# Performance work log

Measured on AMD Instinct MI355X. Metric: run time of the kernel, lower is better.

Reference implementation:

```python
import math
import jax, jax.numpy as jnp
import numpy as np

B, N, D = 16, 4096, 256
N_CAT, N_TPC, N_VPT, N_SP = 16, 8, 4, 16
N_TYPE = N_CAT * N_TPC          # 128
N_VAR = N_TYPE * N_VPT          # 512
THRESH = 0.1
MASK_VAL = jnp.finfo(jnp.float32).min / 2


def _linear(x, w, b):
    # torch nn.Linear: y = x @ W^T + b, W: (out, in)
    return x @ w.T + b


def _level(codes, proj_w, proj_b, K, X, mask, tau):
    """One codebook level: attention of codes over tokens.
    codes: (M, d). Returns H:(B,M,d), w_raw:(B,M)."""
    Q = _linear(codes, proj_w, proj_b)                       # (M, d)
    attn = jnp.einsum('md,bnd->bmn', Q, K) / math.sqrt(D)    # (B, M, N)
    attn = jnp.where(mask[:, None, :], attn, MASK_VAL)
    attn = jnp.clip(attn, -50.0, 50.0)
    G = jnp.nan_to_num(jax.nn.softmax(attn, axis=-1))        # (B, M, N)
    H = jnp.einsum('bmn,bnd->bmd', G, X)                     # (B, M, d)
    w_raw = jnp.linalg.norm(H, axis=-1) / tau                # (B, M)
    return H, w_raw


def _sparsify(w, thr):
    ws = jnp.where(w > thr, w, 0.0)
    return ws / (ws.sum(axis=-1, keepdims=True) + 1e-8)


def _forward(X, positions, category_codes, type_codes, variant_codes,
             spatial_codes, log_tau, cat_w, cat_b, type_w, type_b,
             var_w, var_b, sp_w, sp_b, k_w, k_b, g1_w, g1_b, g2_w, g2_b,
             out_w, out_b, ln_g, ln_b, level_weights, mask):
    tau = jnp.clip(jnp.exp(log_tau[0]) + 0.1, 0.1, 2.0)
    K = _linear(X, k_w, k_b)                                 # (B, N, d)

    # Level 0: category
    H_cat, w_cat_raw = _level(category_codes, cat_w, cat_b, K, X, mask, tau)
    w_cat = jax.nn.softmax(w_cat_raw, axis=-1)
    w_cat_sp = _sparsify(w_cat, THRESH)

    # Level 1: type, gated by category selection
    H_type, w_type_raw = _level(type_codes.reshape(-1, D), type_w, type_b,
                                K, X, mask, tau)
    w_t = (w_type_raw.reshape(-1, N_CAT, N_TPC) * w_cat_sp[:, :, None]
           ).reshape(-1, N_TYPE)
    w_type = jax.nn.softmax(w_t, axis=-1)
    w_type_sp = _sparsify(w_type, THRESH / 2)

    # Level 2: variant, gated by type selection
    H_var, w_var_raw = _level(variant_codes.reshape(-1, D), var_w, var_b,
                              K, X, mask, tau)
    w_type_exp = jnp.repeat(w_type_sp, N_VPT, axis=-1)       # (B, 512)
    w_var = jax.nn.softmax(w_var_raw * w_type_exp, axis=-1)
    w_var_sp = _sparsify(w_var, THRESH / 4)

    # Spatial level (independent)
    H_sp, w_sp_raw = _level(spatial_codes, sp_w, sp_b, K, X, mask, tau)
    w_sp = jax.nn.softmax(w_sp_raw, axis=-1)
    w_sp_sp = _sparsify(w_sp, THRESH)

    z_cat = jnp.einsum('bm,bmd->bd', w_cat_sp, H_cat)
    z_type = jnp.einsum('bm,bmd->bd', w_type_sp, H_type)
    z_var = jnp.einsum('bm,bmd->bd', w_var_sp, H_var)
    z_spatial = jnp.einsum('bm,bmd->bd', w_sp_sp, H_sp)

    # Position gating of category summary
    mask_f = mask.astype(X.dtype)[:, :, None]
    pos_pooled = (positions * mask_f).sum(1) / jnp.maximum(mask_f.sum(1), 1.0)
    gate_in = jnp.concatenate([z_cat, pos_pooled], axis=-1)  # (B, 2d)
    h = jax.nn.gelu(_linear(gate_in, g1_w, g1_b), approximate=False)
    pos_gate = jax.nn.sigmoid(_linear(h, g2_w, g2_b))
    z_cat = z_cat * pos_gate

    # Learned level combine + gated output projection
    lw = jax.nn.softmax(level_weights)
    z = (lw[0] * z_cat + lw[1] * z_type + lw[2] * z_var + lw[3] * z_spatial)
    z = _linear(z, out_w, out_b)
    mu = z.mean(-1, keepdims=True)
    var = z.var(-1, keepdims=True)
    z = (z - mu) / jnp.sqrt(var + 1e-5) * ln_g + ln_b
    return z


def setup_inputs() -> dict:
    key = jax.random.key(0)
    ks = jax.random.split(key, 32)
    s = 1.0 / math.sqrt(D)
    inp = {
        'X': jax.random.normal(ks[0], (B, N, D), jnp.float32),
        'positions': jax.random.normal(ks[1], (B, N, D), jnp.float32),
        'category_codes': jax.random.normal(ks[2], (N_CAT, D)) * 0.02,
        'type_codes': jax.random.normal(ks[3], (N_CAT, N_TPC, D)) * 0.02,
        'variant_codes': jax.random.normal(ks[4], (N_CAT, N_TPC, N_VPT, D)) * 0.02,
        'spatial_codes': jax.random.normal(ks[5], (N_SP, D)) * 0.02,
        'log_tau': jnp.zeros((1,), jnp.float32),
        'cat_w': jax.random.normal(ks[6], (D, D)) * s,
        'cat_b': jnp.zeros((D,)),
        'type_w': jax.random.normal(ks[7], (D, D)) * s,
        'type_b': jnp.zeros((D,)),
        'var_w': jax.random.normal(ks[8], (D, D)) * s,
        'var_b': jnp.zeros((D,)),
        'sp_w': jax.random.normal(ks[9], (D, D)) * s,
        'sp_b': jnp.zeros((D,)),
        'k_w': jax.random.normal(ks[10], (D, D)) * s,
        'k_b': jnp.zeros((D,)),
        'g1_w': jax.random.normal(ks[11], (D, 2 * D)) * s,
        'g1_b': jnp.zeros((D,)),
        'g2_w': jax.random.normal(ks[12], (D, D)) * s,
        'g2_b': jnp.zeros((D,)),
        'out_w': jax.random.normal(ks[13], (D, D)) * s,
        'out_b': jnp.zeros((D,)),
        'ln_g': jnp.ones((D,)),
        'ln_b': jnp.zeros((D,)),
        'level_weights': jnp.ones((4,)) / 4.0,
        'mask': jnp.ones((B, N), jnp.bool_),
    }
    return inp


def reference(X, positions, category_codes, type_codes, variant_codes,
              spatial_codes, log_tau, cat_w, cat_b, type_w, type_b,
              var_w, var_b, sp_w, sp_b, k_w, k_b, g1_w, g1_b, g2_w, g2_b,
              out_w, out_b, ln_g, ln_b, level_weights, mask):
    return _forward(X, positions, category_codes, type_codes, variant_codes,
                    spatial_codes, log_tau, cat_w, cat_b, type_w, type_b,
                    var_w, var_b, sp_w, sp_b, k_w, k_b, g1_w, g1_b,
                    g2_w, g2_b, out_w, out_b, ln_g, ln_b, level_weights, mask)
```

## Files before the change

### kernel.cpp

```cpp
#include <hip/hip_runtime.h>


#define DEV static __device__ __forceinline__

typedef short bf16x8 __attribute__((ext_vector_type(8)));
typedef float f32x4 __attribute__((ext_vector_type(4)));
typedef unsigned short u16x8 __attribute__((ext_vector_type(8)));

DEV float bf2f(unsigned short u) {
  return __uint_as_float(((unsigned int)u) << 16);
}
DEV unsigned short f2bf(float f) {
  unsigned int x = __float_as_uint(f);
  unsigned int r = (x + 0x7fffu + ((x >> 16) & 1u)) >> 16;
  return (unsigned short)r;
}

DEV void gl2lds16(const void* g, void* l) {
  __builtin_amdgcn_global_load_lds(
      (const __attribute__((address_space(1))) unsigned int*)g,
      (__attribute__((address_space(3))) unsigned int*)l, 16, 0, 0);
}

DEV bf16x8 pack8(const float4 a, const float4 b) {
  bf16x8 r;
  r[0] = (short)f2bf(a.x); r[1] = (short)f2bf(a.y);
  r[2] = (short)f2bf(a.z); r[3] = (short)f2bf(a.w);
  r[4] = (short)f2bf(b.x); r[5] = (short)f2bf(b.y);
  r[6] = (short)f2bf(b.z); r[7] = (short)f2bf(b.w);
  return r;
}

DEV size_t pk_off(int rt, int ks) { return ((size_t)rt * 8 + ks) * 512; }

__global__ __launch_bounds__(256) void fused_pre(
    const float* __restrict__ X, const float* __restrict__ k_w,
    const float* __restrict__ k_b, unsigned short* __restrict__ Kp,
    unsigned short* __restrict__ XTp, const float* __restrict__ positions,
    const unsigned char* __restrict__ mask, float* __restrict__ ppart,
    float* __restrict__ cpart, const float* __restrict__ cat_codes,
    const float* __restrict__ type_codes, const float* __restrict__ var_codes,
    const float* __restrict__ sp_codes, const float* __restrict__ cat_w,
    const float* __restrict__ cat_b, const float* __restrict__ type_w,
    const float* __restrict__ type_b, const float* __restrict__ var_w,
    const float* __restrict__ var_b, const float* __restrict__ sp_w,
    const float* __restrict__ sp_b, unsigned short* __restrict__ Qp) {
  __shared__ __align__(16) char smem[36864];
  const int g = blockIdx.x;
  const int t = threadIdx.x;

  if (g < 1024) {
    unsigned short* As = (unsigned short*)smem;
    unsigned short* Bs = (unsigned short*)(smem + 18432);
    const int m0 = (g >> 1) * 128, c0 = (g & 1) * 128;
    const int l = t & 63, w = t >> 6;
    const int wm = (w & 1) * 64, wn = (w >> 1) * 64;
    const f32x4 zero = {0.f, 0.f, 0.f, 0.f};
    f32x4 acc[4][4];
#pragma unroll
    for (int i = 0; i < 4; ++i)
#pragma unroll
      for (int j = 0; j < 4; ++j) acc[i][j] = zero;
    const int rr = t >> 3, cc = (t & 7) * 8;
    for (int kc = 0; kc < 256; kc += 64) {
      __syncthreads();
#pragma unroll
      for (int p = 0; p < 4; ++p) {
        const int r = p * 32 + rr;
        const float* xs = &X[(size_t)(m0 + r) * 256 + kc + cc];
        const float4 a0 = *(const float4*)&xs[0];
        const float4 a1 = *(const float4*)&xs[4];
        *(bf16x8*)&As[r * 72 + cc] = pack8(a0, a1);
        const float* wsrc = &k_w[(size_t)(c0 + r) * 256 + kc + cc];
        const float4 b0 = *(const float4*)&wsrc[0];
        const float4 b1 = *(const float4*)&wsrc[4];
        *(bf16x8*)&Bs[r * 72 + cc] = pack8(b0, b1);
      }
      __syncthreads();
#pragma unroll
      for (int ks = 0; ks < 2; ++ks) {
        const int koff = ks * 32 + ((l >> 4) & 3) * 8;
        bf16x8 a[4], b[4];
#pragma unroll
        for (int f = 0; f < 4; ++f)
          a[f] = *(const bf16x8*)&As[(wm + f * 16 + (l & 15)) * 72 + koff];
#pragma unroll
        for (int f = 0; f < 4; ++f)
          b[f] = *(const bf16x8*)&Bs[(wn + f * 16 + (l & 15)) * 72 + koff];
#pragma unroll
        for (int i = 0; i < 4; ++i)
#pragma unroll
          for (int j = 0; j < 4; ++j)
            acc[i][j] = __builtin_amdgcn_mfma_f32_16x16x32_bf16(
                a[i], b[j], acc[i][j], 0, 0, 0);
      }
    }
    const int q = (l >> 4) & 3;
#pragma unroll
    for (int j = 0; j < 4; ++j) {
      const int c = c0 + wn + j * 16 + (l & 15);
      const float bv = k_b[c];
#pragma unroll
      for (int i = 0; i < 4; ++i) {
        const int mrow = m0 + wm + i * 16 + q * 4;
#pragma unroll
        for (int r = 0; r < 4; ++r) {
          const int m = mrow + r;
          Kp[pk_off(m >> 4, c >> 5) + ((m & 15) + 16 * ((c >> 3) & 3)) * 8 +
             (c & 7)] = f2bf(acc[i][j][r] + bv);
        }
      }
    }
  } else if (g < 5120) {
    float (*Ls)[65] = (float (*)[65])smem;
    const int gg = g - 1024;
    const int b = gg >> 8;
    const int td = (gg >> 6) & 3;
    const int tn = gg & 63;
    const int nl = t >> 2, dp = (t & 3) * 16;
    const float* src =
        X + ((size_t)b * 4096 + tn * 64 + nl) * 256 + td * 64 + dp;
#pragma unroll
    for (int v = 0; v < 4; ++v) {
      const float4 x = *(const float4*)&src[v * 4];
      Ls[nl][dp + v * 4 + 0] = x.x;
      Ls[nl][dp + v * 4 + 1] = x.y;
      Ls[nl][dp + v * 4 + 2] = x.z;
      Ls[nl][dp + v * 4 + 3] = x.w;
    }
    __syncthreads();
    const int dl = t >> 2, np = (t & 3) * 16;
    u16x8 h0, h1;
#pragma unroll
    for (int j = 0; j < 8; ++j) h0[j] = f2bf(Ls[np + j][dl]);
#pragma unroll
    for (int j = 0; j < 8; ++j) h1[j] = f2bf(Ls[np + 8 + j][dl]);
    const int d = td * 64 + dl;
    const int n0g = tn * 64 + np;
    const int n1g = n0g + 8;
    unsigned short* dst = XTp + (size_t)b * 1048576;
    const size_t o0 = (((size_t)(d >> 4) * 128) + (n0g >> 5)) * 512 +
                      ((d & 15) + 16 * ((n0g >> 3) & 3)) * 8;
    const size_t o1 = (((size_t)(d >> 4) * 128) + (n1g >> 5)) * 512 +
                      ((d & 15) + 16 * ((n1g >> 3) & 3)) * 8;
    *(u16x8*)&dst[o0] = h0;
    *(u16x8*)&dst[o1] = h1;
  } else if (g < 5632) {
    float4* red4 = (float4*)smem;
    float* redc = (float*)(smem + 4096);
    const int gg = g - 5120;
    const int b = gg >> 5, seg = gg & 31;
    const int dg = t & 63;
    const int nl = t >> 6;
    const int n0 = seg * 128;
    float4 acc = make_float4(0.f, 0.f, 0.f, 0.f);
    float c = 0.f;
    const float* pb = positions + (size_t)b * 4096 * 256;
    for (int j = 0; j < 32; ++j) {
      const int n = n0 + j * 4 + nl;
      const float mf = mask[(size_t)b * 4096 + n] ? 1.f : 0.f;
      const float4 v = *(const float4*)&pb[(size_t)n * 256 + dg * 4];
      acc.x = fmaf(mf, v.x, acc.x);
      acc.y = fmaf(mf, v.y, acc.y);
      acc.z = fmaf(mf, v.z, acc.z);
      acc.w = fmaf(mf, v.w, acc.w);
      c += mf;
    }
    red4[t] = acc;
    if (dg == 0) redc[nl] = c;
    __syncthreads();
    if (t < 64) {
      float4 s = red4[t];
      const float4 s1 = red4[t + 64], s2 = red4[t + 128], s3 = red4[t + 192];
      s.x += s1.x + s2.x + s3.x;
      s.y += s1.y + s2.y + s3.y;
      s.z += s1.z + s2.z + s3.z;
      s.w += s1.w + s2.w + s3.w;
      *(float4*)&ppart[(size_t)(b * 32 + seg) * 256 + t * 4] = s;
      if (t == 0) cpart[b * 32 + seg] = redc[0] + redc[1] + redc[2] + redc[3];
    }
  } else {
    float* xs = (float*)smem;
    const int m = g - 5632;
    const size_t off = pk_off(m >> 4, t >> 5) +
                       ((m & 15) + 16 * ((t >> 3) & 3)) * 8 + (t & 7);
    if (m >= 672) {
      Qp[off] = 0;
      return;
    }
    const float* code;
    const float* W;
    const float* bias;
    if (m < 16)       { code = cat_codes  + m * 256;         W = cat_w;  bias = cat_b; }
    else if (m < 144) { code = type_codes + (m - 16) * 256;  W = type_w; bias = type_b; }
    else if (m < 656) { code = var_codes  + (m - 144) * 256; W = var_w;  bias = var_b; }
    else              { code = sp_codes   + (m - 656) * 256; W = sp_w;   bias = sp_b; }
    xs[t] = code[t];
    __syncthreads();
    float a = bias[t];
    const float* wr = W + (size_t)t * 256;
    for (int k = 0; k < 256; k += 4) {
      const float4 w = *(const float4*)&wr[k];
      a = fmaf(w.x, xs[k], a);
      a = fmaf(w.y, xs[k + 1], a);
      a = fmaf(w.z, xs[k + 2], a);
      a = fmaf(w.w, xs[k + 3], a);
    }
    Qp[off] = f2bf(a);
  }
}

__global__ __launch_bounds__(256, 2) void attn_fused(
    const unsigned short* __restrict__ Qp, const unsigned short* __restrict__ Kp,
    const unsigned short* __restrict__ XTp,
    const unsigned char* __restrict__ mask, float* __restrict__ H2,
    float* __restrict__ lsum2) {
  __shared__ __align__(16) unsigned short Ks[2][16384];
  __shared__ __align__(16) unsigned short Plds[64 * 72];
  __shared__ unsigned char msk[2048];
  const int combo = blockIdx.x;
  const int m0 = blockIdx.y * 64;
  const int b = combo >> 1;
  const int nsl = combo & 1;
  const int nbase = nsl * 2048;
  const int t = threadIdx.x, l = t & 63, w = t >> 6;
  const int l15 = l & 15, q = l >> 4;
  ((uint2*)msk)[t] = ((const uint2*)(mask + (size_t)b * 4096 + nbase))[t];
  const int mt_g = (m0 >> 4) + w;
  bf16x8 qf[8];
#pragma unroll
  for (int ks = 0; ks < 8; ++ks)
    qf[ks] = *(const bf16x8*)&Qp[pk_off(mt_g, ks) + l * 8];
  const f32x4 zero = {0.f, 0.f, 0.f, 0.f};
  f32x4 accO[4][4];
#pragma unroll
  for (int i = 0; i < 4; ++i)
#pragma unroll
    for (int j = 0; j < 4; ++j) accO[i][j] = zero;
  f32x4 rs = zero;
  const unsigned short* XTb = XTp + (size_t)b * 1048576;
  const unsigned short* Kchunk0 = Kp + ((size_t)b * 256 + (nbase >> 4)) * 4096;
#pragma unroll
  for (int i = 0; i < 8; ++i)
    gl2lds16(Kchunk0 + (w * 8 + i) * 512 + l * 8, &Ks[0][(w * 8 + i) * 512]);
  for (int c = 0; c < 32; ++c) {
    const int cur = c & 1;
    __syncthreads();
    const int nst0 = (nbase >> 5) + c * 2;
    bf16x8 xf[2][4];
#pragma unroll
    for (int ks2 = 0; ks2 < 2; ++ks2)
#pragma unroll
      for (int dj = 0; dj < 4; ++dj)
        xf[ks2][dj] = *(const bf16x8*)&XTb[((size_t)(4 * w + dj) * 128 +
                                            nst0 + ks2) * 512 + l * 8];
    f32x4 accS[4];
#pragma unroll
    for (int f = 0; f < 4; ++f) accS[f] = zero;
#pragma unroll
    for (int ks = 0; ks < 8; ++ks) {
      bf16x8 kf[4];
#pragma unroll
      for (int f = 0; f < 4; ++f)
        kf[f] = *(const bf16x8*)&Ks[cur][(f * 8 + ks) * 512 + l * 8];
#pragma unroll
      for (int f = 0; f < 4; ++f)
        accS[f] = __builtin_amdgcn_mfma_f32_16x16x32_bf16(qf[ks], kf[f],
                                                          accS[f], 0, 0, 0);
    }
#pragma unroll
    for (int f = 0; f < 4; ++f) {
      const bool mk = msk[c * 64 + f * 16 + l15] != 0;
#pragma unroll
      for (int r = 0; r < 4; ++r) {
        float s = accS[f][r] * 0.0625f;
        s = fminf(fmaxf(s, -50.f), 50.f);
        if (!mk) s = -50.f;
        const float e = __expf(s);
        Plds[(w * 16 + q * 4 + r) * 72 + f * 16 + l15] = f2bf(e);
        rs[r] += e;
      }
    }
    __syncthreads();
    if (c < 31) {
      const unsigned short* src = Kchunk0 + (size_t)(c + 1) * 16384;
      unsigned short* dst = &Ks[1 - cur][0];
#pragma unroll
      for (int i = 0; i < 8; ++i)
        gl2lds16(src + (w * 8 + i) * 512 + l * 8, dst + (w * 8 + i) * 512);
    }
#pragma unroll
    for (int ks2 = 0; ks2 < 2; ++ks2) {
      bf16x8 pf[4];
#pragma unroll
      for (int mt = 0; mt < 4; ++mt)
        pf[mt] = *(const bf16x8*)&Plds[(mt * 16 + l15) * 72 + ks2 * 32 + q * 8];
#pragma unroll
      for (int mt = 0; mt < 4; ++mt)
#pragma unroll
        for (int dj = 0; dj < 4; ++dj)
          accO[mt][dj] = __builtin_amdgcn_mfma_f32_16x16x32_bf16(
              pf[mt], xf[ks2][dj], accO[mt][dj], 0, 0, 0);
    }
  }
  float* lpart = lsum2 + (size_t)(nsl * 16 + b) * 672;
#pragma unroll
  for (int r = 0; r < 4; ++r) {
    float v = rs[r];
    v += __shfl_xor(v, 1, 64);
    v += __shfl_xor(v, 2, 64);
    v += __shfl_xor(v, 4, 64);
    v += __shfl_xor(v, 8, 64);
    const int m = m0 + w * 16 + q * 4 + r;
    if (l15 == 0 && m < 672) lpart[m] = v;
  }
  float* Hpart = H2 + (size_t)(nsl * 16 + b) * 672 * 256;
#pragma unroll
  for (int mt = 0; mt < 4; ++mt) {
    const int mbase = m0 + mt * 16 + q * 4;
#pragma unroll
    for (int dj = 0; dj < 4; ++dj) {
      const int d = w * 64 + dj * 16 + l15;
#pragma unroll
      for (int r = 0; r < 4; ++r) {
        const int m = mbase + r;
        if (m < 672) Hpart[(size_t)m * 256 + d] = accO[mt][dj][r];
      }
    }
  }
}

__global__ __launch_bounds__(256) void hnorm_kern(
    const float* __restrict__ H2, const float* __restrict__ lsum2,
    const float* __restrict__ log_tau, float* __restrict__ linv,
    float* __restrict__ wraw) {
  const int b = blockIdx.x, j = blockIdx.y;
  const int t = threadIdx.x, l = t & 63, w = t >> 6;
  const int m = j * 4 + w;
  const size_t r0 = ((size_t)b * 672 + m) * 256;
  const size_t r1 = ((size_t)(16 + b) * 672 + m) * 256;
  const float4 v0 = *(const float4*)&H2[r0 + l * 4];
  const float4 v1 = *(const float4*)&H2[r1 + l * 4];
  const float sx = v0.x + v1.x, sy = v0.y + v1.y;
  const float sz = v0.z + v1.z, sw = v0.w + v1.w;
  float ss = sx * sx + sy * sy + sz * sz + sw * sw;
#pragma unroll
  for (int s = 1; s < 64; s <<= 1) ss += __shfl_xor(ss, s, 64);
  if (l == 0) {
    const float lt = lsum2[b * 672 + m] + lsum2[(16 + b) * 672 + m];
    const float li = 1.0f / lt;
    const float tau = fminf(fmaxf(expf(log_tau[0]) + 0.1f, 0.1f), 2.0f);
    linv[b * 672 + m] = li;
    wraw[b * 672 + m] = sqrtf(ss) * li / tau;
  }
}

DEV float wave_max(float v) {
#pragma unroll
  for (int m = 1; m < 64; m <<= 1) v = fmaxf(v, __shfl_xor(v, m, 64));
  return v;
}
DEV float wave_sum(float v) {
#pragma unroll
  for (int m = 1; m < 64; m <<= 1) v += __shfl_xor(v, m, 64);
  return v;
}

__global__ __launch_bounds__(256) void combine_kern(
    const float* __restrict__ wraw, const float* __restrict__ linv,
    const float* __restrict__ H2, float* __restrict__ zpart) {
  const int b = blockIdx.x, j = blockIdx.y, t = threadIdx.x, l = t & 63;
  __shared__ float wr[672];
  __shared__ float wsp[672];
  for (int i = t; i < 672; i += 256) wr[i] = wraw[b * 672 + i];
  __syncthreads();
  {
    const float v = (l < 16) ? wr[l] : -1e30f;
    const float mx = wave_max(v);
    const float e = (l < 16) ? expf(wr[l] - mx) : 0.f;
    const float s = wave_sum(e);
    float ww = e / s;
    ww = (ww > 0.1f) ? ww : 0.f;
    const float s2 = wave_sum(ww);
    if (l < 16) wsp[l] = ww / (s2 + 1e-8f);
  }
  __syncthreads();
  {
    const float L0 = wr[16 + l] * wsp[l >> 3];
    const float L1 = wr[16 + 64 + l] * wsp[(64 + l) >> 3];
    const float mx = wave_max(fmaxf(L0, L1));
    const float e0 = expf(L0 - mx), e1 = expf(L1 - mx);
    const float s = wave_sum(e0 + e1);
    float w0 = e0 / s, w1 = e1 / s;
    w0 = (w0 > 0.05f) ? w0 : 0.f;
    w1 = (w1 > 0.05f) ? w1 : 0.f;
    const float s2 = wave_sum(w0 + w1);
    const float inv2 = 1.f / (s2 + 1e-8f);
    wsp[16 + l] = w0 * inv2;
    wsp[16 + 64 + l] = w1 * inv2;
  }
  __syncthreads();
  {
    float Lv[8];
    float lm = -1e30f;
#pragma unroll
    for (int jj = 0; jj < 8; ++jj) {
      const int i = l * 8 + jj;
      Lv[jj] = wr[144 + i] * wsp[16 + (i >> 2)];
      lm = fmaxf(lm, Lv[jj]);
    }
    const float mx = wave_max(lm);
    float ls = 0.f;
#pragma unroll
    for (int jj = 0; jj < 8; ++jj) {
      Lv[jj] = expf(Lv[jj] - mx);
      ls += Lv[jj];
    }
    const float s = wave_sum(ls);
    const float inv = 1.f / s;
    float ls2 = 0.f;
#pragma unroll
    for (int jj = 0; jj < 8; ++jj) {
      float ww = Lv[jj] * inv;
      ww = (ww > 0.025f) ? ww : 0.f;
      Lv[jj] = ww;
      ls2 += ww;
    }
    const float s2 = wave_sum(ls2);
    const float inv2 = 1.f / (s2 + 1e-8f);
#pragma unroll
    for (int jj = 0; jj < 8; ++jj) wsp[144 + l * 8 + jj] = Lv[jj] * inv2;
  }
  __syncthreads();
  {
    const float v = (l < 16) ? wr[656 + l] : -1e30f;
    const float mx = wave_max(v);
    const float e = (l < 16) ? expf(wr[656 + l] - mx) : 0.f;
    const float s = wave_sum(e);
    float ww = e / s;
    ww = (ww > 0.1f) ? ww : 0.f;
    const float s2 = wave_sum(ww);
    if (l < 16) wsp[656 + l] = ww / (s2 + 1e-8f);
  }
  __syncthreads();
  for (int i = t; i < 672; i += 256) wsp[i] *= linv[b * 672 + i];
  __syncthreads();
  const float* Ha = H2 + (size_t)b * 672 * 256;
  const float* Hc = H2 + (size_t)(16 + b) * 672 * 256;
  const int s0 = j * 84, s1 = s0 + 84;
  const int Llo[4] = {0, 16, 144, 656};
  const int Lhi[4] = {16, 144, 656, 672};
#pragma unroll
  for (int lv = 0; lv < 4; ++lv) {
    const int lo = max(s0, Llo[lv]);
    const int hi = min(s1, Lhi[lv]);
    float z = 0.f;
    for (int m = lo; m < hi; ++m)
      z = fmaf(wsp[m], Ha[(size_t)m * 256 + t] + Hc[(size_t)m * 256 + t], z);
    zpart[(((size_t)b * 8 + j) * 4 + lv) * 256 + t] = z;
  }
}

__global__ __launch_bounds__(1024) void gate_kern(
    const float* __restrict__ zpart, const float* __restrict__ ppart,
    const float* __restrict__ cpart, const float* __restrict__ g1_w,
    const float* __restrict__ g1_b, const float* __restrict__ g2_w,
    const float* __restrict__ g2_b, const float* __restrict__ out_w,
    const float* __restrict__ out_b, const float* __restrict__ ln_g,
    const float* __restrict__ ln_b, const float* __restrict__ lvlw,
    float* __restrict__ out) {
  const int b = blockIdx.x, t = threadIdx.x;
  __shared__ float gin[512];
  __shared__ float zvs[4][256];
  __shared__ float hb[256];
  __shared__ float zc[256];
  __shared__ float oar[256];
  __shared__ float red[256];
  __shared__ float par[1024];
  __shared__ float cred;
  {
    const int lv = t >> 8, tt = t & 255;
    float z = 0.f;
#pragma unroll
    for (int jj = 0; jj < 8; ++jj)
      z += zpart[(((size_t)b * 8 + jj) * 4 + lv) * 256 + tt];
    zvs[lv][tt] = z;
  }
  if (t == 0) {
    float c = 0.f;
    for (int seg = 0; seg < 32; ++seg) c += cpart[b * 32 + seg];
    cred = fmaxf(c, 1.0f);
  }
  __syncthreads();
  if (t < 256) {
    float pa = 0.f;
    for (int seg = 0; seg < 32; ++seg)
      pa += ppart[(size_t)(b * 32 + seg) * 256 + t];
    gin[256 + t] = pa / cred;
    gin[t] = zvs[0][t];
  }
  __syncthreads();
  {
    const int r = t >> 2, p = t & 3;
    const float* w1 = g1_w + (size_t)r * 512 + p * 128;
    const float* gv = gin + p * 128;
    float a = 0.f;
    for (int k = 0; k < 128; k += 4) {
      const float4 w = *(const float4*)&w1[k];
      a = fmaf(w.x, gv[k], a);
      a = fmaf(w.y, gv[k + 1], a);
      a = fmaf(w.z, gv[k + 2], a);
      a = fmaf(w.w, gv[k + 3], a);
    }
    par[t] = a;
  }
  __syncthreads();
  if (t < 256) {
    const float a =
        par[t * 4] + par[t * 4 + 1] + par[t * 4 + 2] + par[t * 4 + 3] +
        g1_b[t];
    hb[t] = 0.5f * a * (1.0f + erff(a * 0.7071067811865475f));
  }
  __syncthreads();
  {
    const int r = t >> 2, p = t & 3;
    const float* w2 = g2_w + (size_t)r * 256 + p * 64;
    const float* hv = hb + p * 64;
    float a = 0.f;
    for (int k = 0; k < 64; k += 4) {
      const float4 w = *(const float4*)&w2[k];
      a = fmaf(w.x, hv[k], a);
      a = fmaf(w.y, hv[k + 1], a);
      a = fmaf(w.z, hv[k + 2], a);
      a = fmaf(w.w, hv[k + 3], a);
    }
    par[t] = a;
  }
  __syncthreads();
  if (t < 256) {
    const float a2 =
        par[t * 4] + par[t * 4 + 1] + par[t * 4 + 2] + par[t * 4 + 3] +
        g2_b[t];
    const float pg = 1.0f / (1.0f + expf(-a2));
    const float l0 = lvlw[0], l1 = lvlw[1], l2 = lvlw[2], l3 = lvlw[3];
    const float mx = fmaxf(fmaxf(l0, l1), fmaxf(l2, l3));
    const float e0 = expf(l0 - mx), e1 = expf(l1 - mx);
    const float e2 = expf(l2 - mx), e3 = expf(l3 - mx);
    const float einv = 1.0f / (e0 + e1 + e2 + e3);
    zc[t] = (e0 * zvs[0][t] * pg + e1 * zvs[1][t] + e2 * zvs[2][t] +
             e3 * zvs[3][t]) *
            einv;
  }
  __syncthreads();
  {
    const int r = t >> 2, p = t & 3;
    const float* wo = out_w + (size_t)r * 256 + p * 64;
    const float* zv = zc + p * 64;
    float a = 0.f;
    for (int k = 0; k < 64; k += 4) {
      const float4 w = *(const float4*)&wo[k];
      a = fmaf(w.x, zv[k], a);
      a = fmaf(w.y, zv[k + 1], a);
      a = fmaf(w.z, zv[k + 2], a);
      a = fmaf(w.w, zv[k + 3], a);
    }
    par[t] = a;
  }
  __syncthreads();
  if (t < 256) {
    const float o =
        par[t * 4] + par[t * 4 + 1] + par[t * 4 + 2] + par[t * 4 + 3] +
        out_b[t];
    oar[t] = o;
    red[t] = o;
  }
  __syncthreads();
  for (int s = 128; s > 0; s >>= 1) {
    if (t < s) red[t] += red[t + s];
    __syncthreads();
  }
  const float mu = red[0] / 256.f;
  __syncthreads();
  if (t < 256) red[t] = oar[t] * oar[t];
  __syncthreads();
  for (int s = 128; s > 0; s >>= 1) {
    if (t < s) red[t] += red[t + s];
    __syncthreads();
  }
  if (t < 256) {
    const float var = red[0] / 256.f - mu * mu;
    out[b * 256 + t] = (oar[t] - mu) * rsqrtf(var + 1e-5f) * ln_g[t] + ln_b[t];
  }
}

extern "C" void kernel_launch(void* const* d_in, const int* in_sizes, int n_in,
                              void* d_out, int out_size, void* d_ws,
                              size_t ws_size, hipStream_t stream) {
  (void)in_sizes; (void)n_in; (void)out_size; (void)ws_size;
  const float* X          = (const float*)d_in[0];
  const float* positions  = (const float*)d_in[1];
  const float* cat_codes  = (const float*)d_in[2];
  const float* type_codes = (const float*)d_in[3];
  const float* var_codes  = (const float*)d_in[4];
  const float* sp_codes   = (const float*)d_in[5];
  const float* log_tau    = (const float*)d_in[6];
  const float* cat_w      = (const float*)d_in[7];
  const float* cat_b      = (const float*)d_in[8];
  const float* type_w     = (const float*)d_in[9];
  const float* type_b     = (const float*)d_in[10];
  const float* var_w      = (const float*)d_in[11];
  const float* var_b      = (const float*)d_in[12];
  const float* sp_w       = (const float*)d_in[13];
  const float* sp_b       = (const float*)d_in[14];
  const float* k_w        = (const float*)d_in[15];
  const float* k_b        = (const float*)d_in[16];
  const float* g1_w       = (const float*)d_in[17];
  const float* g1_b       = (const float*)d_in[18];
  const float* g2_w       = (const float*)d_in[19];
  const float* g2_b       = (const float*)d_in[20];
  const float* out_w      = (const float*)d_in[21];
  const float* out_b      = (const float*)d_in[22];
  const float* ln_g       = (const float*)d_in[23];
  const float* ln_b       = (const float*)d_in[24];
  const float* lvlw       = (const float*)d_in[25];
  const unsigned char* mask = (const unsigned char*)d_in[26];

  char* ws = (char*)d_ws;
  constexpr size_t O_KP  = 0;
  constexpr size_t O_XT  = 33554432;
  constexpr size_t O_QP  = 67108864;
  constexpr size_t O_H2  = 67469312;
  constexpr size_t O_L2  = 89489408;
  constexpr size_t O_PP  = 89575424;
  constexpr size_t O_CP  = 90099712;
  constexpr size_t O_ZP  = 90101760;
  constexpr size_t O_LI  = 90626048;
  constexpr size_t O_WR  = 90669056;

  unsigned short* Kp  = (unsigned short*)(ws + O_KP);
  unsigned short* XTp = (unsigned short*)(ws + O_XT);
  unsigned short* Qp  = (unsigned short*)(ws + O_QP);
  float* H2           = (float*)(ws + O_H2);
  float* lsum2        = (float*)(ws + O_L2);
  float* ppart        = (float*)(ws + O_PP);
  float* cpart        = (float*)(ws + O_CP);
  float* zpart        = (float*)(ws + O_ZP);
  float* linv         = (float*)(ws + O_LI);
  float* wraw         = (float*)(ws + O_WR);
  float* out          = (float*)d_out;

  fused_pre<<<dim3(6336), 256, 0, stream>>>(
      X, k_w, k_b, Kp, XTp, positions, mask, ppart, cpart, cat_codes,
      type_codes, var_codes, sp_codes, cat_w, cat_b, type_w, type_b, var_w,
      var_b, sp_w, sp_b, Qp);

  attn_fused<<<dim3(32, 11), 256, 0, stream>>>(Qp, Kp, XTp, mask, H2, lsum2);

  hnorm_kern<<<dim3(16, 168), 256, 0, stream>>>(H2, lsum2, log_tau, linv,
                                                wraw);

  combine_kern<<<dim3(16, 8), 256, 0, stream>>>(wraw, linv, H2, zpart);

  gate_kern<<<dim3(16), 1024, 0, stream>>>(zpart, ppart, cpart, g1_w, g1_b,
                                           g2_w, g2_b, out_w, out_b, ln_g,
                                           ln_b, lvlw, out);
}
```

Baseline: 383.0 us.

## Load K-projection operands directly to registers; widen combine grid; parallelize ppart reduction

The K-projection GEMM branch of fused_pre drops its LDS staging and barriers: each lane now reads its MFMA fragments straight from global memory and converts them to bf16 in registers. The shared buffer shrinks to match, which may allow more blocks per CU. combine_kern runs 32 slices per batch instead of 8, with the zpart buffer and workspace offsets enlarged to fit. gate_kern now splits the ppart reduction across all 1024 threads. The price is redundant global reads across waves in the GEMM and more partial sums to reduce afterwards.

```diff
diff --git a/kernel.cpp b/kernel.cpp
--- a/kernel.cpp
+++ b/kernel.cpp
@@ -45,60 +45,49 @@
     const float* __restrict__ type_b, const float* __restrict__ var_w,
     const float* __restrict__ var_b, const float* __restrict__ sp_w,
     const float* __restrict__ sp_b, unsigned short* __restrict__ Qp) {
-  __shared__ __align__(16) char smem[36864];
+  __shared__ __align__(16) char smem[16640];
   const int g = blockIdx.x;
   const int t = threadIdx.x;
 
   if (g < 1024) {
-    unsigned short* As = (unsigned short*)smem;
-    unsigned short* Bs = (unsigned short*)(smem + 18432);
     const int m0 = (g >> 1) * 128, c0 = (g & 1) * 128;
     const int l = t & 63, w = t >> 6;
     const int wm = (w & 1) * 64, wn = (w >> 1) * 64;
+    const int l15 = l & 15, q8 = ((l >> 4) & 3) * 8;
+    const float* ax[4];
+    const float* bx[4];
+#pragma unroll
+    for (int f = 0; f < 4; ++f) {
+      ax[f] = X + (size_t)(m0 + wm + f * 16 + l15) * 256;
+      bx[f] = k_w + (size_t)(c0 + wn + f * 16 + l15) * 256;
+    }
     const f32x4 zero = {0.f, 0.f, 0.f, 0.f};
     f32x4 acc[4][4];
 #pragma unroll
     for (int i = 0; i < 4; ++i)
 #pragma unroll
       for (int j = 0; j < 4; ++j) acc[i][j] = zero;
-    const int rr = t >> 3, cc = (t & 7) * 8;
-    for (int kc = 0; kc < 256; kc += 64) {
-      __syncthreads();
-#pragma unroll
-      for (int p = 0; p < 4; ++p) {
-        const int r = p * 32 + rr;
-        const float* xs = &X[(size_t)(m0 + r) * 256 + kc + cc];
-        const float4 a0 = *(const float4*)&xs[0];
-        const float4 a1 = *(const float4*)&xs[4];
-        *(bf16x8*)&As[r * 72 + cc] = pack8(a0, a1);
-        const float* wsrc = &k_w[(size_t)(c0 + r) * 256 + kc + cc];
-        const float4 b0 = *(const float4*)&wsrc[0];
-        const float4 b1 = *(const float4*)&wsrc[4];
-        *(bf16x8*)&Bs[r * 72 + cc] = pack8(b0, b1);
-      }
-      __syncthreads();
-#pragma unroll
-      for (int ks = 0; ks < 2; ++ks) {
-        const int koff = ks * 32 + ((l >> 4) & 3) * 8;
-        bf16x8 a[4], b[4];
-#pragma unroll
-        for (int f = 0; f < 4; ++f)
-          a[f] = *(const bf16x8*)&As[(wm + f * 16 + (l & 15)) * 72 + koff];
-#pragma unroll
-        for (int f = 0; f < 4; ++f)
-          b[f] = *(const bf16x8*)&Bs[(wn + f * 16 + (l & 15)) * 72 + koff];
-#pragma unroll
-        for (int i = 0; i < 4; ++i)
-#pragma unroll
-          for (int j = 0; j < 4; ++j)
-            acc[i][j] = __builtin_amdgcn_mfma_f32_16x16x32_bf16(
-                a[i], b[j], acc[i][j], 0, 0, 0);
-      }
+#pragma unroll
+    for (int kc = 0; kc < 256; kc += 32) {
+      const int ko = kc + q8;
+      bf16x8 a[4], b[4];
+#pragma unroll
+      for (int f = 0; f < 4; ++f)
+        a[f] = pack8(*(const float4*)&ax[f][ko], *(const float4*)&ax[f][ko + 4]);
+#pragma unroll
+      for (int f = 0; f < 4; ++f)
+        b[f] = pack8(*(const float4*)&bx[f][ko], *(const float4*)&bx[f][ko + 4]);
+#pragma unroll
+      for (int i = 0; i < 4; ++i)
+#pragma unroll
+        for (int j = 0; j < 4; ++j)
+          acc[i][j] = __builtin_amdgcn_mfma_f32_16x16x32_bf16(
+              a[i], b[j], acc[i][j], 0, 0, 0);
     }
     const int q = (l >> 4) & 3;
 #pragma unroll
     for (int j = 0; j < 4; ++j) {
-      const int c = c0 + wn + j * 16 + (l & 15);
+      const int c = c0 + wn + j * 16 + l15;
       const float bv = k_b[c];
 #pragma unroll
       for (int i = 0; i < 4; ++i) {
@@ -447,7 +436,7 @@
   __syncthreads();
   const float* Ha = H2 + (size_t)b * 672 * 256;
   const float* Hc = H2 + (size_t)(16 + b) * 672 * 256;
-  const int s0 = j * 84, s1 = s0 + 84;
+  const int s0 = j * 21, s1 = s0 + 21;
   const int Llo[4] = {0, 16, 144, 656};
   const int Lhi[4] = {16, 144, 656, 672};
 #pragma unroll
@@ -457,7 +446,7 @@
     float z = 0.f;
     for (int m = lo; m < hi; ++m)
       z = fmaf(wsp[m], Ha[(size_t)m * 256 + t] + Hc[(size_t)m * 256 + t], z);
-    zpart[(((size_t)b * 8 + j) * 4 + lv) * 256 + t] = z;
+    zpart[(((size_t)b * 32 + j) * 4 + lv) * 256 + t] = z;
   }
 }
 
@@ -482,9 +471,17 @@
     const int lv = t >> 8, tt = t & 255;
     float z = 0.f;
 #pragma unroll
-    for (int jj = 0; jj < 8; ++jj)
-      z += zpart[(((size_t)b * 8 + jj) * 4 + lv) * 256 + tt];
+    for (int jj = 0; jj < 32; ++jj)
+      z += zpart[(((size_t)b * 32 + jj) * 4 + lv) * 256 + tt];
     zvs[lv][tt] = z;
+  }
+  {
+    const int p = t >> 8, tt = t & 255;
+    float pa = 0.f;
+#pragma unroll
+    for (int s = 0; s < 8; ++s)
+      pa += ppart[(size_t)(b * 32 + p * 8 + s) * 256 + tt];
+    par[t] = pa;
   }
   if (t == 0) {
     float c = 0.f;
@@ -493,9 +490,7 @@
   }
   __syncthreads();
   if (t < 256) {
-    float pa = 0.f;
-    for (int seg = 0; seg < 32; ++seg)
-      pa += ppart[(size_t)(b * 32 + seg) * 256 + t];
+    const float pa = par[t] + par[256 + t] + par[512 + t] + par[768 + t];
     gin[256 + t] = pa / cred;
     gin[t] = zvs[0][t];
   }
@@ -634,8 +629,8 @@
   constexpr size_t O_PP  = 89575424;
   constexpr size_t O_CP  = 90099712;
   constexpr size_t O_ZP  = 90101760;
-  constexpr size_t O_LI  = 90626048;
-  constexpr size_t O_WR  = 90669056;
+  constexpr size_t O_LI  = 92198912;
+  constexpr size_t O_WR  = 92241920;
 
   unsigned short* Kp  = (unsigned short*)(ws + O_KP);
   unsigned short* XTp = (unsigned short*)(ws + O_XT);
@@ -659,7 +654,7 @@
   hnorm_kern<<<dim3(16, 168), 256, 0, stream>>>(H2, lsum2, log_tau, linv,
                                                 wraw);
 
-  combine_kern<<<dim3(16, 8), 256, 0, stream>>>(wraw, linv, H2, zpart);
+  combine_kern<<<dim3(16, 32), 256, 0, stream>>>(wraw, linv, H2, zpart);
 
   gate_kern<<<dim3(16), 1024, 0, stream>>>(zpart, ppart, cpart, g1_w, g1_b,
                                            g2_w, g2_b, out_w, out_b, ln_g,
```

Result: slower. 412.7 us (+7.7%).
